# Kernel optimization log

Hardware: AMD Instinct MI355X
Metric: run time of the kernel (lower is better)

The kernel has to match this reference:

```python
import jax, jax.numpy as jnp
import numpy as np
import math

EPS_RMS = 1.1920929e-07  # torch nn.RMSNorm default eps = finfo(float32).eps
EPS_DEN = 1e-6


def rmsnorm(x, gamma):
    ms = jnp.mean(x * x, axis=-1, keepdims=True)
    return x * jax.lax.rsqrt(ms + EPS_RMS) * gamma


def setup_inputs() -> dict:
    key = jax.random.key(0)
    ks = jax.random.split(key, 8)
    B, T, K, D = 4, 4096, 256, 1024
    x_tokens = jax.random.normal(ks[0], (B, T, D), dtype=jnp.float32)
    ctx = jax.random.normal(ks[1], (B, K, D), dtype=jnp.float32)
    idx = jnp.sort(jax.random.randint(ks[2], (B, T), 0, K), axis=-1)
    s = 1.0 / math.sqrt(D)
    Wq = jax.random.normal(ks[3], (D, D), dtype=jnp.float32) * s
    Wk = jax.random.normal(ks[4], (D, D), dtype=jnp.float32) * s
    Wv = jax.random.normal(ks[5], (D, D), dtype=jnp.float32) * s
    Wo = jax.random.normal(ks[6], (D, D), dtype=jnp.float32) * s
    return {
        'x_tokens': x_tokens, 'ctx': ctx, 'ctx_index_per_token': idx,
        'gamma_q': jnp.ones((D,), jnp.float32), 'gamma_kv': jnp.ones((D,), jnp.float32),
        'Wq': Wq, 'Wk': Wk, 'Wv': Wv, 'Wo': Wo,
    }


def reference(x_tokens, ctx, ctx_index_per_token, gamma_q, gamma_kv, Wq, Wk, Wv, Wo):
    B, T, D = x_tokens.shape
    K = ctx.shape[1]
    H = 16
    hd = D // H

    def split(x):  # (B,S,D) -> (B,H,S,hd)
        return x.reshape(B, -1, H, hd).transpose(0, 2, 1, 3)

    q = split(rmsnorm(x_tokens, gamma_q) @ Wq.T)
    kn = rmsnorm(ctx, gamma_kv)
    k = split(kn @ Wk.T)
    v = split(kn @ Wv.T)

    # band mask: |ctx_pos - idx| <= 1, shape (B,1,T,K)
    ctx_pos = jnp.arange(K)[None, None, :]
    mask = (jnp.abs(ctx_pos - ctx_index_per_token[:, :, None]) <= 1)[:, None]

    scores = jnp.einsum('bhqd,bhkd->bhqk', q, k) / math.sqrt(hd)
    w = jnp.square(jax.nn.relu(scores))
    w = jnp.where(mask, w, 0.0)
    denom = jnp.maximum(w.sum(-1, keepdims=True), EPS_DEN)
    out = jnp.einsum('bhqk,bhkd->bhqd', w / denom, v)
    out = out.transpose(0, 2, 1, 3).reshape(B, T, D)
    return x_tokens + out @ Wo.T
```

## Files before the change

kernel.cpp:

```cpp
#include <hip/hip_runtime.h>
#include <hip/hip_bf16.h>
#include <stdint.h>

#define D_DIM 1024

using f32x4  = __attribute__((ext_vector_type(4))) float;
using short8 = __attribute__((ext_vector_type(8))) short;

__device__ __forceinline__ float bf2f(unsigned short u) {
    union { unsigned int i; float f; } v; v.i = ((unsigned int)u) << 16; return v.f;
}
__device__ __forceinline__ unsigned short f2bf(float f) {
    union { float f; unsigned int i; } v; v.f = f;
    unsigned int x = v.i;
    return (unsigned short)((x + 0x7fffu + ((x >> 16) & 1u)) >> 16);
}
__device__ __forceinline__ void gload16(const void* g, void* l) {
    __builtin_amdgcn_global_load_lds(
        (const __attribute__((address_space(1))) void*)g,
        (__attribute__((address_space(3))) void*)l, 16, 0, 0);
}

__global__ __launch_bounds__(256)
void convw_kernel(const float* __restrict__ Wk, const float* __restrict__ Wv,
                  const float* __restrict__ Wo, const float* __restrict__ gkv,
                  unsigned short* __restrict__ wk_hi, unsigned short* __restrict__ wk_lo,
                  unsigned short* __restrict__ wv_hi, unsigned short* __restrict__ wv_lo,
                  unsigned short* __restrict__ wo_b)
{
    const int e   = (blockIdx.x * 256 + threadIdx.x) * 4;
    const int sel = e >> 20;
    const int off = e & 0xFFFFF;
    const float* src = sel == 0 ? Wk : sel == 1 ? Wv : Wo;
    float4 v = *(const float4*)(src + off);
    if (sel < 2) {
        float4 g = *(const float4*)(gkv + (off & 1023));
        v.x *= g.x; v.y *= g.y; v.z *= g.z; v.w *= g.w;
        ushort4 h, l;
        h.x = f2bf(v.x); l.x = f2bf(v.x - bf2f(h.x));
        h.y = f2bf(v.y); l.y = f2bf(v.y - bf2f(h.y));
        h.z = f2bf(v.z); l.z = f2bf(v.z - bf2f(h.z));
        h.w = f2bf(v.w); l.w = f2bf(v.w - bf2f(h.w));
        unsigned short* hi = sel == 0 ? wk_hi : wv_hi;
        unsigned short* lo = sel == 0 ? wk_lo : wv_lo;
        *(ushort4*)(hi + off) = h;
        *(ushort4*)(lo + off) = l;
    } else {
        ushort4 o;
        o.x = f2bf(v.x); o.y = f2bf(v.y); o.z = f2bf(v.z); o.w = f2bf(v.w);
        *(ushort4*)(wo_b + off) = o;
    }
}

__global__ __launch_bounds__(256)
void transq_kernel(const float* __restrict__ Wq, const float* __restrict__ gq,
                   unsigned short* __restrict__ th, unsigned short* __restrict__ tl)
{
    __shared__ float tile[64][65];
    const int c0 = (blockIdx.x & 15) * 64;
    const int i0 = (blockIdx.x >> 4) * 64;
    const int tid = threadIdx.x;
#pragma unroll
    for (int j = 0; j < 4; ++j) {
        const int e  = tid + j * 256;
        const int rl = e >> 4;
        const int q4 = e & 15;
        float4 v = *(const float4*)(Wq + (long)(c0 + rl) * 1024 + i0 + q4 * 4);
        tile[q4 * 4 + 0][rl] = v.x;
        tile[q4 * 4 + 1][rl] = v.y;
        tile[q4 * 4 + 2][rl] = v.z;
        tile[q4 * 4 + 3][rl] = v.w;
    }
    __syncthreads();
#pragma unroll
    for (int j = 0; j < 4; ++j) {
        const int e  = tid + j * 256;
        const int il = e >> 4;
        const int s4 = e & 15;
        const float g = gq[i0 + il];
        float v0 = tile[il][s4 * 4 + 0] * g;
        float v1 = tile[il][s4 * 4 + 1] * g;
        float v2 = tile[il][s4 * 4 + 2] * g;
        float v3 = tile[il][s4 * 4 + 3] * g;
        ushort4 hh, ll;
        hh.x = f2bf(v0); ll.x = f2bf(v0 - bf2f(hh.x));
        hh.y = f2bf(v1); ll.y = f2bf(v1 - bf2f(hh.y));
        hh.z = f2bf(v2); ll.z = f2bf(v2 - bf2f(hh.z));
        hh.w = f2bf(v3); ll.w = f2bf(v3 - bf2f(hh.w));
        const long o = (long)(i0 + il) * 1024 + c0 + s4 * 4;
        *(ushort4*)(th + o) = hh;
        *(ushort4*)(tl + o) = ll;
    }
}

__global__ __launch_bounds__(256)
void rms_split_kernel(const float* __restrict__ x,
                      unsigned short* __restrict__ xh, unsigned short* __restrict__ xl)
{
    const long row = blockIdx.x;
    float4 v = ((const float4*)(x + row * D_DIM))[threadIdx.x];
    float ss = v.x*v.x + v.y*v.y + v.z*v.z + v.w*v.w;
#pragma unroll
    for (int m = 32; m; m >>= 1) ss += __shfl_xor(ss, m);
    __shared__ float red[4];
    if ((threadIdx.x & 63) == 0) red[threadIdx.x >> 6] = ss;
    __syncthreads();
    const float tot = red[0] + red[1] + red[2] + red[3];
    const float scale = rsqrtf(tot * (1.0f / 1024.0f) + 1.1920929e-07f);
    v.x *= scale; v.y *= scale; v.z *= scale; v.w *= scale;
    ushort4 h, l;
    h.x = f2bf(v.x); l.x = f2bf(v.x - bf2f(h.x));
    h.y = f2bf(v.y); l.y = f2bf(v.y - bf2f(h.y));
    h.z = f2bf(v.z); l.z = f2bf(v.z - bf2f(h.z));
    h.w = f2bf(v.w); l.w = f2bf(v.w - bf2f(h.w));
    *(ushort4*)(xh + row * D_DIM + threadIdx.x * 4) = h;
    *(ushort4*)(xl + row * D_DIM + threadIdx.x * 4) = l;
}

__global__ __launch_bounds__(256)
void gemm_kv(const unsigned short* __restrict__ ch, const unsigned short* __restrict__ cl,
             const unsigned short* __restrict__ wkh, const unsigned short* __restrict__ wkl,
             const unsigned short* __restrict__ wvh,
             unsigned short* __restrict__ kh, unsigned short* __restrict__ kl,
             float* __restrict__ v_f)
{
    __shared__ unsigned short Ah[4096], Al[4096], Bh[4096], Bl[4096];
    const bool full = (blockIdx.z == 0);
    const unsigned short* Bhp = full ? wkh : wvh;
    const unsigned short* Blp = wkl;

    const int tid = threadIdx.x, lane = tid & 63, wave = tid >> 6;
    const int wm = wave >> 1, wn = wave & 1;
    const long Arow0 = (long)blockIdx.y * 128;
    const int  Brow0 = blockIdx.x * 128;
    const int fr = lane & 15, ks = lane >> 4;
    const int ksz = (ks ^ ((fr >> 1) & 3)) << 4;
    const int kq  = ((tid & 3) ^ ((tid >> 3) & 3)) * 8;
    const int srow = tid >> 2;

    const long a_off0 = (Arow0 + srow) * D_DIM + kq;
    const long a_off1 = (Arow0 + srow + 64) * D_DIM + kq;
    const long b_off0 = (long)(Brow0 + srow) * D_DIM + kq;
    const long b_off1 = (long)(Brow0 + srow + 64) * D_DIM + kq;

    f32x4 acc[4][4] = {};
    char* AhB = (char*)Ah; char* AlB = (char*)Al;
    char* BhB = (char*)Bh; char* BlB = (char*)Bl;

    for (int kt = 0; kt < 32; ++kt) {
        const int k0 = kt * 32;
        gload16(ch + a_off0 + k0, AhB + tid * 16);
        gload16(ch + a_off1 + k0, AhB + 4096 + tid * 16);
        gload16(Bhp + b_off0 + k0, BhB + tid * 16);
        gload16(Bhp + b_off1 + k0, BhB + 4096 + tid * 16);
        if (full) {
            gload16(cl + a_off0 + k0, AlB + tid * 16);
            gload16(cl + a_off1 + k0, AlB + 4096 + tid * 16);
            gload16(Blp + b_off0 + k0, BlB + tid * 16);
            gload16(Blp + b_off1 + k0, BlB + 4096 + tid * 16);
        }
        __syncthreads();

        short8 ah[4], al[4], bh[4], bl[4];
#pragma unroll
        for (int mi = 0; mi < 4; ++mi) {
            const int aoff = (wm * 64 + mi * 16 + fr) * 64 + ksz;
            ah[mi] = *(const short8*)(AhB + aoff);
            if (full) al[mi] = *(const short8*)(AlB + aoff);
        }
#pragma unroll
        for (int ni = 0; ni < 4; ++ni) {
            const int boff = (wn * 64 + ni * 16 + fr) * 64 + ksz;
            bh[ni] = *(const short8*)(BhB + boff);
            if (full) bl[ni] = *(const short8*)(BlB + boff);
        }
#pragma unroll
        for (int mi = 0; mi < 4; ++mi)
#pragma unroll
            for (int ni = 0; ni < 4; ++ni) {
                acc[mi][ni] = __builtin_amdgcn_mfma_f32_16x16x32_bf16(ah[mi], bh[ni], acc[mi][ni], 0, 0, 0);
                if (full) {
                    acc[mi][ni] = __builtin_amdgcn_mfma_f32_16x16x32_bf16(al[mi], bh[ni], acc[mi][ni], 0, 0, 0);
                    acc[mi][ni] = __builtin_amdgcn_mfma_f32_16x16x32_bf16(ah[mi], bl[ni], acc[mi][ni], 0, 0, 0);
                }
            }
        __syncthreads();
    }

    const int c = lane & 15, r0 = (lane >> 4) * 4;
#pragma unroll
    for (int mi = 0; mi < 4; ++mi)
#pragma unroll
        for (int ni = 0; ni < 4; ++ni)
#pragma unroll
            for (int j = 0; j < 4; ++j) {
                const long row = Arow0 + wm * 64 + mi * 16 + r0 + j;
                const int  col = Brow0 + wn * 64 + ni * 16 + c;
                const float val = acc[mi][ni][j];
                if (full) {
                    const unsigned short hh = f2bf(val);
                    kh[row * D_DIM + col] = hh;
                    kl[row * D_DIM + col] = f2bf(val - bf2f(hh));
                } else {
                    v_f[row * D_DIM + col] = val;
                }
            }
}

__global__ __launch_bounds__(256)
void gemm_U(const unsigned short* __restrict__ kh, const unsigned short* __restrict__ kl,
            const unsigned short* __restrict__ th, const unsigned short* __restrict__ tl,
            unsigned short* __restrict__ Uh, unsigned short* __restrict__ Ul)
{
    __shared__ unsigned short Ah[4096], Al[4096], Bh[4096], Bl[4096];
    const int h = blockIdx.z;
    const int tid = threadIdx.x, lane = tid & 63, wave = tid >> 6;
    const int wm = wave >> 1, wn = wave & 1;
    const long Arow0 = (long)blockIdx.y * 128;
    const int  Brow0 = blockIdx.x * 128;
    const int fr = lane & 15, ks = lane >> 4;
    const int ksz = (ks ^ ((fr >> 1) & 3)) << 4;
    const int kq  = ((tid & 3) ^ ((tid >> 3) & 3)) * 8;
    const int srow = tid >> 2;
    const int kb = h * 64;

    const long a_off0 = (Arow0 + srow) * D_DIM + kb + kq;
    const long a_off1 = (Arow0 + srow + 64) * D_DIM + kb + kq;
    const long b_off0 = (long)(Brow0 + srow) * D_DIM + kb + kq;
    const long b_off1 = (long)(Brow0 + srow + 64) * D_DIM + kb + kq;

    f32x4 acc[4][4] = {};
    char* AhB = (char*)Ah; char* AlB = (char*)Al;
    char* BhB = (char*)Bh; char* BlB = (char*)Bl;

    for (int kt = 0; kt < 2; ++kt) {
        const int k0 = kt * 32;
        gload16(kh + a_off0 + k0, AhB + tid * 16);
        gload16(kh + a_off1 + k0, AhB + 4096 + tid * 16);
        gload16(kl + a_off0 + k0, AlB + tid * 16);
        gload16(kl + a_off1 + k0, AlB + 4096 + tid * 16);
        gload16(th + b_off0 + k0, BhB + tid * 16);
        gload16(th + b_off1 + k0, BhB + 4096 + tid * 16);
        gload16(tl + b_off0 + k0, BlB + tid * 16);
        gload16(tl + b_off1 + k0, BlB + 4096 + tid * 16);
        __syncthreads();

        short8 ah[4], al[4], bh[4], bl[4];
#pragma unroll
        for (int mi = 0; mi < 4; ++mi) {
            const int aoff = (wm * 64 + mi * 16 + fr) * 64 + ksz;
            ah[mi] = *(const short8*)(AhB + aoff);
            al[mi] = *(const short8*)(AlB + aoff);
        }
#pragma unroll
        for (int ni = 0; ni < 4; ++ni) {
            const int boff = (wn * 64 + ni * 16 + fr) * 64 + ksz;
            bh[ni] = *(const short8*)(BhB + boff);
            bl[ni] = *(const short8*)(BlB + boff);
        }
#pragma unroll
        for (int mi = 0; mi < 4; ++mi)
#pragma unroll
            for (int ni = 0; ni < 4; ++ni) {
                acc[mi][ni] = __builtin_amdgcn_mfma_f32_16x16x32_bf16(ah[mi], bh[ni], acc[mi][ni], 0, 0, 0);
                acc[mi][ni] = __builtin_amdgcn_mfma_f32_16x16x32_bf16(al[mi], bh[ni], acc[mi][ni], 0, 0, 0);
                acc[mi][ni] = __builtin_amdgcn_mfma_f32_16x16x32_bf16(ah[mi], bl[ni], acc[mi][ni], 0, 0, 0);
            }
        __syncthreads();
    }

    const int c = lane & 15, r0 = (lane >> 4) * 4;
#pragma unroll
    for (int mi = 0; mi < 4; ++mi)
#pragma unroll
        for (int ni = 0; ni < 4; ++ni)
#pragma unroll
            for (int j = 0; j < 4; ++j) {
                const long row = Arow0 + wm * 64 + mi * 16 + r0 + j;
                const int  col = Brow0 + wn * 64 + ni * 16 + c;
                const float val = acc[mi][ni][j];
                const long o = ((long)row * 16 + h) * 1024 + col;
                const unsigned short hh = f2bf(val);
                Uh[o] = hh;
                Ul[o] = f2bf(val - bf2f(hh));
            }
}

__global__ __launch_bounds__(256)
void score_gemm(const float* __restrict__ x, const int* __restrict__ cidx,
                const unsigned short* __restrict__ Uh, const unsigned short* __restrict__ Ul,
                float* __restrict__ sbuf)
{
    const int pg = blockIdx.x;
    const int mh = blockIdx.y;
    const int b  = blockIdx.z;
    const int p0 = pg * 4;
    const int* ci = cidx + (b << 12);
    int l = 0, r = 4096;
    while (l < r) { int m = (l + r) >> 1; if (ci[m] < p0 - 1) l = m + 1; else r = m; }
    const int lo = l;
    r = 4096;
    while (l < r) { int m = (l + r) >> 1; if (ci[m] <= p0 + 4) l = m + 1; else r = m; }
    const int hi = l;
    if (lo + mh * 64 >= hi) return;

    __shared__ unsigned short AhS[2][2048], AlS[2][2048];
    __shared__ unsigned short UhS[2][2048], UlS[2][2048];
    __shared__ float scl[64];

    const int tid = threadIdx.x, lane = tid & 63, wave = tid >> 6;
    const int fr = lane & 15;
    const int ks = lane >> 4;
    const int ksz = (ks ^ ((fr >> 1) & 3)) << 4;

    const int arow = tid >> 2, aq = tid & 3;
    const int aslot = aq ^ ((arow >> 1) & 3);
    const unsigned short* const Uhb = Uh + ((long)((b << 8) + p0) * 16) * 1024;
    const unsigned short* const Ulb = Ul + ((long)((b << 8) + p0) * 16) * 1024;
    const float* const xb = x + ((long)b << 12) * 1024;

    for (int t0 = lo + mh * 64; t0 < hi; t0 += 128) {
        const int tc0 = (t0 + arow < hi) ? (t0 + arow) : (hi - 1);
        const float* xr = xb + (long)tc0 * 1024 + aq * 8;
        float ss = 0.f;

        gload16(Uhb + (long)arow * 1024 + aslot * 8, (char*)&UhS[0][0] + tid * 16);
        gload16(Ulb + (long)arow * 1024 + aslot * 8, (char*)&UlS[0][0] + tid * 16);
        {
            const float4 v0 = *(const float4*)(xr);
            const float4 v1 = *(const float4*)(xr + 4);
            ss += v0.x*v0.x + v0.y*v0.y + v0.z*v0.z + v0.w*v0.w
                + v1.x*v1.x + v1.y*v1.y + v1.z*v1.z + v1.w*v1.w;
            short8 hv, lv;
            unsigned short h_;
            h_ = f2bf(v0.x); hv[0] = (short)h_; lv[0] = (short)f2bf(v0.x - bf2f(h_));
            h_ = f2bf(v0.y); hv[1] = (short)h_; lv[1] = (short)f2bf(v0.y - bf2f(h_));
            h_ = f2bf(v0.z); hv[2] = (short)h_; lv[2] = (short)f2bf(v0.z - bf2f(h_));
            h_ = f2bf(v0.w); hv[3] = (short)h_; lv[3] = (short)f2bf(v0.w - bf2f(h_));
            h_ = f2bf(v1.x); hv[4] = (short)h_; lv[4] = (short)f2bf(v1.x - bf2f(h_));
            h_ = f2bf(v1.y); hv[5] = (short)h_; lv[5] = (short)f2bf(v1.y - bf2f(h_));
            h_ = f2bf(v1.z); hv[6] = (short)h_; lv[6] = (short)f2bf(v1.z - bf2f(h_));
            h_ = f2bf(v1.w); hv[7] = (short)h_; lv[7] = (short)f2bf(v1.w - bf2f(h_));
            *(short8*)((char*)&AhS[0][0] + arow * 64 + aslot * 16) = hv;
            *(short8*)((char*)&AlS[0][0] + arow * 64 + aslot * 16) = lv;
        }
        __syncthreads();

        f32x4 acc[4] = {};
        for (int t = 0; t < 32; ++t) {
            const int cur = t & 1, nxt = cur ^ 1;
            float4 v0, v1;
            if (t < 31) {
                const int k0n = (t + 1) * 32;
                gload16(Uhb + (long)arow * 1024 + k0n + aslot * 8, (char*)&UhS[nxt][0] + tid * 16);
                gload16(Ulb + (long)arow * 1024 + k0n + aslot * 8, (char*)&UlS[nxt][0] + tid * 16);
                v0 = *(const float4*)(xr + k0n);
                v1 = *(const float4*)(xr + k0n + 4);
            }

            const int aoff = cur * 4096 + (wave * 16 + fr) * 64 + ksz;
            const short8 ah = *(const short8*)((char*)&AhS[0][0] + aoff);
            const short8 al = *(const short8*)((char*)&AlS[0][0] + aoff);
#pragma unroll
            for (int ni = 0; ni < 4; ++ni) {
                const int boff = cur * 4096 + (ni * 16 + fr) * 64 + ksz;
                const short8 uh = *(const short8*)((char*)&UhS[0][0] + boff);
                const short8 ul = *(const short8*)((char*)&UlS[0][0] + boff);
                acc[ni] = __builtin_amdgcn_mfma_f32_16x16x32_bf16(ah, uh, acc[ni], 0, 0, 0);
                acc[ni] = __builtin_amdgcn_mfma_f32_16x16x32_bf16(al, uh, acc[ni], 0, 0, 0);
                acc[ni] = __builtin_amdgcn_mfma_f32_16x16x32_bf16(ah, ul, acc[ni], 0, 0, 0);
            }

            if (t < 31) {
                ss += v0.x*v0.x + v0.y*v0.y + v0.z*v0.z + v0.w*v0.w
                    + v1.x*v1.x + v1.y*v1.y + v1.z*v1.z + v1.w*v1.w;
                short8 hv, lv;
                unsigned short h_;
                h_ = f2bf(v0.x); hv[0] = (short)h_; lv[0] = (short)f2bf(v0.x - bf2f(h_));
                h_ = f2bf(v0.y); hv[1] = (short)h_; lv[1] = (short)f2bf(v0.y - bf2f(h_));
                h_ = f2bf(v0.z); hv[2] = (short)h_; lv[2] = (short)f2bf(v0.z - bf2f(h_));
                h_ = f2bf(v0.w); hv[3] = (short)h_; lv[3] = (short)f2bf(v0.w - bf2f(h_));
                h_ = f2bf(v1.x); hv[4] = (short)h_; lv[4] = (short)f2bf(v1.x - bf2f(h_));
                h_ = f2bf(v1.y); hv[5] = (short)h_; lv[5] = (short)f2bf(v1.y - bf2f(h_));
                h_ = f2bf(v1.z); hv[6] = (short)h_; lv[6] = (short)f2bf(v1.z - bf2f(h_));
                h_ = f2bf(v1.w); hv[7] = (short)h_; lv[7] = (short)f2bf(v1.w - bf2f(h_));
                *(short8*)((char*)&AhS[0][0] + nxt * 4096 + arow * 64 + aslot * 16) = hv;
                *(short8*)((char*)&AlS[0][0] + nxt * 4096 + arow * 64 + aslot * 16) = lv;
            }
            __syncthreads();
        }

        ss += __shfl_xor(ss, 1);
        ss += __shfl_xor(ss, 2);
        if (aq == 0) scl[arow] = rsqrtf(ss * (1.0f / 1024.0f) + 1.1920929e-07f);
        __syncthreads();

        const int hcol = lane & 15;
        const int r0j = (lane >> 4) * 4;
#pragma unroll
        for (int j = 0; j < 4; ++j) {
            const int trow = t0 + wave * 16 + r0j + j;
            if (trow < hi) {
                const float sscale = scl[wave * 16 + r0j + j] * 0.125f;
                const long tg = ((long)b << 12) + trow;
                const int idx = ci[trow];
#pragma unroll
                for (int ni = 0; ni < 4; ++ni) {
                    const int dp = p0 + ni - idx + 1;
                    if (dp >= 0 && dp <= 2)
                        sbuf[(tg * 16 + hcol) * 3 + dp] = acc[ni][j] * sscale;
                }
            }
        }
        __syncthreads();
    }
}

__global__ __launch_bounds__(256)
void attnout_kernel(const float* __restrict__ sbuf, const float* __restrict__ vf,
                    const int* __restrict__ cidx, unsigned short* __restrict__ ao)
{
    const int tid = threadIdx.x;
    const int tg = tid >> 4, h = tid & 15;
    const int t = blockIdx.x * 16 + tg;
    const int b = t >> 12;
    const int idx = cidx[t];
    const float* sb = sbuf + ((long)t * 16 + h) * 3;
    float w0 = 0.f, w1 = 0.f, w2 = 0.f, wsum = 0.f;
    if (idx - 1 >= 0) { float s = sb[0]; if (s > 0.f) { w0 = s * s; wsum += w0; } }
    { float s = sb[1]; if (s > 0.f) { w1 = s * s; wsum += w1; } }
    if (idx + 1 < 256) { float s = sb[2]; if (s > 0.f) { w2 = s * s; wsum += w2; } }
    const float inv = 1.0f / fmaxf(wsum, 1e-6f);
    w0 *= inv; w1 *= inv; w2 *= inv;
    const int p0 = idx > 0 ? idx - 1 : 0;
    const int p2 = idx < 255 ? idx + 1 : 255;
    const float4* v0 = (const float4*)(vf + ((long)(b * 256 + p0)) * 1024 + h * 64);
    const float4* v1 = (const float4*)(vf + ((long)(b * 256 + idx)) * 1024 + h * 64);
    const float4* v2 = (const float4*)(vf + ((long)(b * 256 + p2)) * 1024 + h * 64);
    ushort4* aop = (ushort4*)(ao + (long)t * 1024 + h * 64);
#pragma unroll
    for (int q = 0; q < 16; ++q) {
        float4 a0 = v0[q], a1 = v1[q], a2 = v2[q];
        ushort4 o;
        o.x = f2bf(w0 * a0.x + w1 * a1.x + w2 * a2.x);
        o.y = f2bf(w0 * a0.y + w1 * a1.y + w2 * a2.y);
        o.z = f2bf(w0 * a0.z + w1 * a1.z + w2 * a2.z);
        o.w = f2bf(w0 * a0.w + w1 * a1.w + w2 * a2.w);
        aop[q] = o;
    }
}

__global__ __launch_bounds__(512, 2)
void gemm_out256(const unsigned short* __restrict__ A,
                 const unsigned short* __restrict__ W,
                 float* __restrict__ C, const float* __restrict__ resid)
{
    __shared__ unsigned short As[2][8192];
    __shared__ unsigned short Bs[2][8192];

    const int lin = blockIdx.x;
    const int bx = (lin >> 3) & 3;
    const int by = ((lin >> 5) << 3) | (lin & 7);
    const long row0 = (long)by * 256;
    const int  col0 = bx * 256;

    const int tid = threadIdx.x, lane = tid & 63, wave = tid >> 6;
    const int wm = wave >> 2, wn = wave & 3;
    const int fr = lane & 15, ks = lane >> 4;
    const int ksz = (ks ^ ((fr >> 1) & 3)) << 4;
    const int kq  = ((tid & 3) ^ ((tid >> 3) & 3)) * 8;
    const int srow = tid >> 2;

    const long a_off0 = (row0 + srow) * D_DIM + kq;
    const long a_off1 = (row0 + 128 + srow) * D_DIM + kq;
    const long b_off0 = (long)(col0 + srow) * D_DIM + kq;
    const long b_off1 = (long)(col0 + 128 + srow) * D_DIM + kq;

    f32x4 acc[8][4] = {};

    gload16(A + a_off0, (char*)&As[0][0] + tid * 16);
    gload16(A + a_off1, (char*)&As[0][0] + 8192 + tid * 16);
    gload16(W + b_off0, (char*)&Bs[0][0] + tid * 16);
    gload16(W + b_off1, (char*)&Bs[0][0] + 8192 + tid * 16);
    __syncthreads();

    int cur = 0;
    for (int t = 0; t < 32; ++t) {
        const int nxt = cur ^ 1;
        if (t < 31) {
            const int k0 = (t + 1) * 32;
            gload16(A + a_off0 + k0, (char*)&As[nxt][0] + tid * 16);
            gload16(A + a_off1 + k0, (char*)&As[nxt][0] + 8192 + tid * 16);
            gload16(W + b_off0 + k0, (char*)&Bs[nxt][0] + tid * 16);
            gload16(W + b_off1 + k0, (char*)&Bs[nxt][0] + 8192 + tid * 16);
        }

        short8 bfrag[4];
#pragma unroll
        for (int ni = 0; ni < 4; ++ni)
            bfrag[ni] = *(const short8*)((char*)&Bs[cur][0] + (wn * 64 + ni * 16 + fr) * 64 + ksz);
#pragma unroll
        for (int mi = 0; mi < 8; ++mi) {
            const short8 a = *(const short8*)((char*)&As[cur][0] + (wm * 128 + mi * 16 + fr) * 64 + ksz);
#pragma unroll
            for (int ni = 0; ni < 4; ++ni)
                acc[mi][ni] = __builtin_amdgcn_mfma_f32_16x16x32_bf16(a, bfrag[ni], acc[mi][ni], 0, 0, 0);
        }
        __syncthreads();
        cur = nxt;
    }

    const int c = lane & 15, rg = lane >> 4;
#pragma unroll
    for (int mi = 0; mi < 8; ++mi)
#pragma unroll
        for (int ni = 0; ni < 4; ++ni)
#pragma unroll
            for (int j = 0; j < 4; ++j) {
                const long row = row0 + wm * 128 + mi * 16 + rg * 4 + j;
                const int  col = col0 + wn * 64 + ni * 16 + c;
                C[row * D_DIM + col] = resid[row * D_DIM + col] + acc[mi][ni][j];
            }
}

extern "C" void kernel_launch(void* const* d_in, const int* in_sizes, int n_in,
                              void* d_out, int out_size, void* d_ws, size_t ws_size,
                              hipStream_t stream)
{
    const float* x    = (const float*)d_in[0];
    const float* ctx  = (const float*)d_in[1];
    const int*   cidx = (const int*)d_in[2];
    const float* gq   = (const float*)d_in[3];
    const float* gkv  = (const float*)d_in[4];
    const float* Wq   = (const float*)d_in[5];
    const float* Wk   = (const float*)d_in[6];
    const float* Wv   = (const float*)d_in[7];
    const float* Wo   = (const float*)d_in[8];
    float* out = (float*)d_out;

    char* ws = (char*)d_ws;
    const size_t MB = 1 << 20;
    unsigned short* wqT_hi = (unsigned short*)(ws + 0 * MB);
    unsigned short* wqT_lo = (unsigned short*)(ws + 2 * MB);
    unsigned short* wk_hi  = (unsigned short*)(ws + 4 * MB);
    unsigned short* wk_lo  = (unsigned short*)(ws + 6 * MB);
    unsigned short* wv_hi  = (unsigned short*)(ws + 8 * MB);
    unsigned short* wv_lo  = (unsigned short*)(ws + 10 * MB);
    unsigned short* wo_b   = (unsigned short*)(ws + 12 * MB);
    unsigned short* ch = (unsigned short*)(ws + 14 * MB);
    unsigned short* cl = (unsigned short*)(ws + 16 * MB);
    unsigned short* kh = (unsigned short*)(ws + 18 * MB);
    unsigned short* kl = (unsigned short*)(ws + 20 * MB);
    float* v_f = (float*)(ws + 22 * MB);
    unsigned short* Uh = (unsigned short*)(ws + 26 * MB);
    unsigned short* Ul = (unsigned short*)(ws + 58 * MB);
    unsigned short* ao_b = (unsigned short*)(ws + 26 * MB);
    float* sbuf = (float*)(ws + 91 * MB);

    convw_kernel<<<3072, 256, 0, stream>>>(Wk, Wv, Wo, gkv,
                                           wk_hi, wk_lo, wv_hi, wv_lo, wo_b);
    transq_kernel<<<256, 256, 0, stream>>>(Wq, gq, wqT_hi, wqT_lo);
    rms_split_kernel<<<1024, 256, 0, stream>>>(ctx, ch, cl);
    gemm_kv<<<dim3(8, 8, 2), 256, 0, stream>>>(ch, cl, wk_hi, wk_lo, wv_hi,
                                               kh, kl, v_f);
    gemm_U<<<dim3(8, 8, 16), 256, 0, stream>>>(kh, kl, wqT_hi, wqT_lo, Uh, Ul);
    score_gemm<<<dim3(64, 2, 4), 256, 0, stream>>>(x, cidx, Uh, Ul, sbuf);
    attnout_kernel<<<1024, 256, 0, stream>>>(sbuf, v_f, cidx, ao_b);
    gemm_out256<<<256, 512, 0, stream>>>(ao_b, wo_b, out, x);
}
```

Measured before the change: 210.2 us.

## Split score GEMM reduction dimension in two and combine partials in attnout

New measurement: 202.3 us. -3.7%, faster.

```diff
diff --git a/kernel.cpp b/kernel.cpp
--- a/kernel.cpp
+++ b/kernel.cpp
@@ -289,11 +289,14 @@
 __global__ __launch_bounds__(256)
 void score_gemm(const float* __restrict__ x, const int* __restrict__ cidx,
                 const unsigned short* __restrict__ Uh, const unsigned short* __restrict__ Ul,
-                float* __restrict__ sbuf)
+                float* __restrict__ sbuf, float* __restrict__ ssbuf)
 {
     const int pg = blockIdx.x;
     const int mh = blockIdx.y;
-    const int b  = blockIdx.z;
+    const int bz = blockIdx.z;
+    const int b  = bz & 3;
+    const int ksp = bz >> 2;
+    const int kbase = ksp << 9;
     const int p0 = pg * 4;
     const int* ci = cidx + (b << 12);
     int l = 0, r = 4096;
@@ -304,9 +307,11 @@
     const int hi = l;
     if (lo + mh * 64 >= hi) return;
 
+    float* const sb = sbuf + (long)ksp * 786432;
+    float* const ssb = ssbuf + (ksp << 14);
+
     __shared__ unsigned short AhS[2][2048], AlS[2][2048];
     __shared__ unsigned short UhS[2][2048], UlS[2][2048];
-    __shared__ float scl[64];
 
     const int tid = threadIdx.x, lane = tid & 63, wave = tid >> 6;
     const int fr = lane & 15;
@@ -315,9 +320,9 @@
 
     const int arow = tid >> 2, aq = tid & 3;
     const int aslot = aq ^ ((arow >> 1) & 3);
-    const unsigned short* const Uhb = Uh + ((long)((b << 8) + p0) * 16) * 1024;
-    const unsigned short* const Ulb = Ul + ((long)((b << 8) + p0) * 16) * 1024;
-    const float* const xb = x + ((long)b << 12) * 1024;
+    const unsigned short* const Uhb = Uh + ((long)((b << 8) + p0) * 16) * 1024 + kbase;
+    const unsigned short* const Ulb = Ul + ((long)((b << 8) + p0) * 16) * 1024 + kbase;
+    const float* const xb = x + ((long)b << 12) * 1024 + kbase;
 
     for (int t0 = lo + mh * 64; t0 < hi; t0 += 128) {
         const int tc0 = (t0 + arow < hi) ? (t0 + arow) : (hi - 1);
@@ -347,10 +352,10 @@
         __syncthreads();
 
         f32x4 acc[4] = {};
-        for (int t = 0; t < 32; ++t) {
+        for (int t = 0; t < 16; ++t) {
             const int cur = t & 1, nxt = cur ^ 1;
             float4 v0, v1;
-            if (t < 31) {
+            if (t < 15) {
                 const int k0n = (t + 1) * 32;
                 gload16(Uhb + (long)arow * 1024 + k0n + aslot * 8, (char*)&UhS[nxt][0] + tid * 16);
                 gload16(Ulb + (long)arow * 1024 + k0n + aslot * 8, (char*)&UlS[nxt][0] + tid * 16);
@@ -371,7 +376,7 @@
                 acc[ni] = __builtin_amdgcn_mfma_f32_16x16x32_bf16(ah, ul, acc[ni], 0, 0, 0);
             }
 
-            if (t < 31) {
+            if (t < 15) {
                 ss += v0.x*v0.x + v0.y*v0.y + v0.z*v0.z + v0.w*v0.w
                     + v1.x*v1.x + v1.y*v1.y + v1.z*v1.z + v1.w*v1.w;
                 short8 hv, lv;
@@ -392,8 +397,8 @@
 
         ss += __shfl_xor(ss, 1);
         ss += __shfl_xor(ss, 2);
-        if (aq == 0) scl[arow] = rsqrtf(ss * (1.0f / 1024.0f) + 1.1920929e-07f);
-        __syncthreads();
+        if (aq == 0 && t0 + arow < hi)
+            ssb[(b << 12) + t0 + arow] = ss;
 
         const int hcol = lane & 15;
         const int r0j = (lane >> 4) * 4;
@@ -401,14 +406,13 @@
         for (int j = 0; j < 4; ++j) {
             const int trow = t0 + wave * 16 + r0j + j;
             if (trow < hi) {
-                const float sscale = scl[wave * 16 + r0j + j] * 0.125f;
                 const long tg = ((long)b << 12) + trow;
                 const int idx = ci[trow];
 #pragma unroll
                 for (int ni = 0; ni < 4; ++ni) {
                     const int dp = p0 + ni - idx + 1;
                     if (dp >= 0 && dp <= 2)
-                        sbuf[(tg * 16 + hcol) * 3 + dp] = acc[ni][j] * sscale;
+                        sb[(tg * 16 + hcol) * 3 + dp] = acc[ni][j];
                 }
             }
         }
@@ -417,19 +421,23 @@
 }
 
 __global__ __launch_bounds__(256)
-void attnout_kernel(const float* __restrict__ sbuf, const float* __restrict__ vf,
-                    const int* __restrict__ cidx, unsigned short* __restrict__ ao)
+void attnout_kernel(const float* __restrict__ sbuf, const float* __restrict__ ssbuf,
+                    const float* __restrict__ vf, const int* __restrict__ cidx,
+                    unsigned short* __restrict__ ao)
 {
     const int tid = threadIdx.x;
     const int tg = tid >> 4, h = tid & 15;
     const int t = blockIdx.x * 16 + tg;
     const int b = t >> 12;
     const int idx = cidx[t];
-    const float* sb = sbuf + ((long)t * 16 + h) * 3;
+    const float* sb0 = sbuf + ((long)t * 16 + h) * 3;
+    const float* sb1 = sb0 + 786432;
+    const float ssum = ssbuf[t] + ssbuf[t + 16384];
+    const float scale = rsqrtf(ssum * (1.0f / 1024.0f) + 1.1920929e-07f) * 0.125f;
     float w0 = 0.f, w1 = 0.f, w2 = 0.f, wsum = 0.f;
-    if (idx - 1 >= 0) { float s = sb[0]; if (s > 0.f) { w0 = s * s; wsum += w0; } }
-    { float s = sb[1]; if (s > 0.f) { w1 = s * s; wsum += w1; } }
-    if (idx + 1 < 256) { float s = sb[2]; if (s > 0.f) { w2 = s * s; wsum += w2; } }
+    if (idx - 1 >= 0) { float s = (sb0[0] + sb1[0]) * scale; if (s > 0.f) { w0 = s * s; wsum += w0; } }
+    { float s = (sb0[1] + sb1[1]) * scale; if (s > 0.f) { w1 = s * s; wsum += w1; } }
+    if (idx + 1 < 256) { float s = (sb0[2] + sb1[2]) * scale; if (s > 0.f) { w2 = s * s; wsum += w2; } }
     const float inv = 1.0f / fmaxf(wsum, 1e-6f);
     w0 *= inv; w1 *= inv; w2 *= inv;
     const int p0 = idx > 0 ? idx - 1 : 0;
@@ -555,7 +563,8 @@
     unsigned short* Uh = (unsigned short*)(ws + 26 * MB);
     unsigned short* Ul = (unsigned short*)(ws + 58 * MB);
     unsigned short* ao_b = (unsigned short*)(ws + 26 * MB);
-    float* sbuf = (float*)(ws + 91 * MB);
+    float* sbuf  = (float*)(ws + 91 * MB);
+    float* ssbuf = (float*)(ws + 97 * MB);
 
     convw_kernel<<<3072, 256, 0, stream>>>(Wk, Wv, Wo, gkv,
                                            wk_hi, wk_lo, wv_hi, wv_lo, wo_b);
@@ -564,7 +573,7 @@
     gemm_kv<<<dim3(8, 8, 2), 256, 0, stream>>>(ch, cl, wk_hi, wk_lo, wv_hi,
                                                kh, kl, v_f);
     gemm_U<<<dim3(8, 8, 16), 256, 0, stream>>>(kh, kl, wqT_hi, wqT_lo, Uh, Ul);
-    score_gemm<<<dim3(64, 2, 4), 256, 0, stream>>>(x, cidx, Uh, Ul, sbuf);
-    attnout_kernel<<<1024, 256, 0, stream>>>(sbuf, v_f, cidx, ao_b);
+    score_gemm<<<dim3(64, 2, 8), 256, 0, stream>>>(x, cidx, Uh, Ul, sbuf, ssbuf);
+    attnout_kernel<<<1024, 256, 0, stream>>>(sbuf, ssbuf, v_f, cidx, ao_b);
     gemm_out256<<<256, 512, 0, stream>>>(ao_b, wo_b, out, x);
 }
```
